# Optimization experiments

Hardware: AMD Instinct MI355X
Metric: run time of the kernel (lower is better)

Reference implementation:

```python
import jax, jax.numpy as jnp
import numpy as np

EPS = 1e-5  # torch BatchNorm2d default eps

def _bn_train(x, g, b):
    # BatchNorm2d in training mode: batch statistics over (N, H, W), biased variance
    m = x.mean(axis=(0, 2, 3), keepdims=True)
    v = x.var(axis=(0, 2, 3), keepdims=True)
    return g[None, :, None, None] * (x - m) / jnp.sqrt(v + EPS) + b[None, :, None, None]

def _conv3(x, w, b):
    y = jax.lax.conv_general_dilated(x, w, (1, 1), 'SAME',
                                     dimension_numbers=('NCHW', 'OIHW', 'NCHW'))
    return y + b[None, :, None, None]

def _conv1(x, w, b):
    # 1x1 conv == per-pixel matmul; w: [out, in]
    return jnp.einsum('bchw,oc->bohw', x, w) + b[None, :, None, None]

def _projector(x, w1, b1, g1, be1, w2, b2, g2, be2):
    h = jax.nn.relu(_bn_train(_conv3(x, w1, b1), g1, be1))
    return _bn_train(_conv1(h, w2, b2), g2, be2)

def _cross_teacher_attention(s, teachers, wq, bq, wk, bk, wv, bv):
    B, C, H, W = s.shape
    scale = C ** -0.5
    q = _conv1(s, wq, bq).reshape(B, C, H * W).transpose(0, 2, 1)  # [B, HW, C]
    outs, ws = [], []
    for t in teachers:  # small fixed list of teachers (structural branch)
        k = _conv1(t, wk, bk).reshape(B, C, H * W).transpose(0, 2, 1)
        v = _conv1(t, wv, bv).reshape(B, C, H * W).transpose(0, 2, 1)
        a = jax.nn.softmax(jnp.einsum('bqc,bkc->bqk', q, k) * scale, axis=-1)  # [B, HW, HW]
        outs.append(jnp.einsum('bqk,bkc->bqc', a, v))                          # [B, HW, C]
        ws.append(a.mean(axis=-1))                                             # [B, HW]
    w = jax.nn.softmax(jnp.stack(ws, axis=-1), axis=-1)          # [B, HW, T]
    fused = jnp.einsum('bqt,tbqc->bqc', w, jnp.stack(outs, 0))   # weighted sum over teachers
    fused = fused.reshape(B, H, W, C).transpose(0, 3, 1, 2)      # [B, C, H, W]
    return s + fused

def setup_inputs() -> dict:
    key = jax.random.key(0)
    ks = jax.random.split(key, 16)
    B, C, H, W = 8, 128, 56, 56
    T = 256  # teacher projector output dim
    d = {}
    d['student_mid'] = jax.random.normal(ks[0], (B, C, H, W), jnp.float32)
    d['t1_mid'] = jax.random.normal(ks[1], (B, C, H, W), jnp.float32)
    d['t2_mid'] = jax.random.normal(ks[2], (B, C, H, W), jnp.float32)
    for i, n in enumerate(['q', 'k', 'v']):
        d['w' + n] = jax.random.normal(ks[3 + i], (C, C), jnp.float32) * 0.05
        d['b' + n] = jnp.zeros((C,), jnp.float32)
    for p, off in (('p1', 6), ('p2', 10)):
        d[p + '_w1'] = jax.random.normal(ks[off], (C, C, 3, 3), jnp.float32) * 0.05
        d[p + '_b1'] = jnp.zeros((C,), jnp.float32)
        d[p + '_g1'] = jnp.ones((C,), jnp.float32)
        d[p + '_be1'] = jnp.zeros((C,), jnp.float32)
        d[p + '_w2'] = jax.random.normal(ks[off + 1], (T, C), jnp.float32) * 0.05
        d[p + '_b2'] = jnp.zeros((T,), jnp.float32)
        d[p + '_g2'] = jnp.ones((T,), jnp.float32)
        d[p + '_be2'] = jnp.zeros((T,), jnp.float32)
    return d

def reference(student_mid, t1_mid, t2_mid, wq, bq, wk, bk, wv, bv,
              p1_w1, p1_b1, p1_g1, p1_be1, p1_w2, p1_b2, p1_g2, p1_be2,
              p2_w1, p2_b1, p2_g1, p2_be1, p2_w2, p2_b2, p2_g2, p2_be2):
    # Per-teacher projectors: computed by the torch module but their outputs are
    # never consumed by the attention (s_feat_proj is unused) -> dead code.
    _sp1 = _projector(student_mid, p1_w1, p1_b1, p1_g1, p1_be1, p1_w2, p1_b2, p1_g2, p1_be2)
    _sp2 = _projector(student_mid, p2_w1, p2_b1, p2_g1, p2_be1, p2_w2, p2_b2, p2_g2, p2_be2)
    del _sp1, _sp2
    return _cross_teacher_attention(student_mid, [t1_mid, t2_mid], wq, bq, wk, bk, wv, bv)
```

## Files before the change

kernel.cpp:

```cpp
#include <hip/hip_runtime.h>

#define HW 3136
#define NB 8
#define CD 128
#define QSCALE 0.12751750206f

typedef __attribute__((ext_vector_type(8))) short short8;
typedef __attribute__((ext_vector_type(4))) float floatx4;
typedef __attribute__((ext_vector_type(4))) unsigned short ushort4v;

static __device__ __forceinline__ unsigned short f2b(float f){
  union { float f; unsigned u; } v; v.f = f;
  unsigned r = v.u + 0x7FFFu + ((v.u >> 16) & 1u);
  return (unsigned short)(r >> 16);
}
static __device__ __forceinline__ float b2f(unsigned short h){
  union { unsigned u; float f; } v; v.u = ((unsigned)h) << 16;
  return v.f;
}

__global__ __launch_bounds__(256) void proj_kernel(
    const float* __restrict__ s, const float* __restrict__ t1, const float* __restrict__ t2,
    const float* __restrict__ wq, const float* __restrict__ bq,
    const float* __restrict__ wk, const float* __restrict__ bk,
    const float* __restrict__ wv, const float* __restrict__ bv,
    unsigned short* __restrict__ qkv)
{
  __shared__ __align__(16) unsigned short WL[CD][136];
  __shared__ __align__(16) unsigned short xsT[64][136];
  const int job = blockIdx.z;
  const float* x; const float* w; const float* bias; float scl; int cmajor; size_t dstoff;
  switch(job){
    case 0: x=s;  w=wq; bias=bq; scl=QSCALE; cmajor=0; dstoff=0; break;
    case 1: x=t1; w=wk; bias=bk; scl=1.f;    cmajor=0; dstoff=1; break;
    case 2: x=t1; w=wv; bias=bv; scl=1.f;    cmajor=1; dstoff=2; break;
    case 3: x=t2; w=wk; bias=bk; scl=1.f;    cmajor=0; dstoff=3; break;
    default:x=t2; w=wv; bias=bv; scl=1.f;    cmajor=1; dstoff=4; break;
  }
  const size_t TS = (size_t)NB*HW*CD;
  const int b   = blockIdx.y;
  const int hw0 = blockIdx.x * 64;
  const int tid = threadIdx.x;

  for (int i = 0; i < 16; i++){
    int flat = tid + i*256;
    int o = flat >> 5, cq = (flat & 31)*4;
    floatx4 wv4 = *(const floatx4*)(w + (size_t)o*CD + cq);
    ushort4v pk;
    for (int j=0;j<4;j++) pk[j] = f2b(wv4[j]);
    *(ushort4v*)&WL[o][cq] = pk;
  }
  const float* xb = x + (size_t)b*CD*HW + hw0;
  for (int i = 0; i < 8; i++){
    int flat = (tid + i*256)*4;
    int c = flat >> 6, hh = flat & 63;
    floatx4 xv = *(const floatx4*)(xb + (size_t)c*HW + hh);
    for (int j=0;j<4;j++) xsT[hh+j][c] = f2b(xv[j]);
  }
  __syncthreads();

  const int m = tid & 15, quad = (tid >> 4) & 3, wv_ = tid >> 6;
  short8 af[4];
  for (int dk=0;dk<4;dk++)
    af[dk] = *(const short8*)&xsT[wv_*16 + m][dk*32 + quad*8];
  float bb[8];
  for (int nt=0;nt<8;nt++) bb[nt] = bias[nt*16 + m];

  unsigned short* dstK = qkv + dstoff*TS + ((size_t)b*HW + hw0)*CD;
  unsigned short* dstV = qkv + dstoff*TS + (size_t)b*CD*HW;
  for (int nt=0;nt<8;nt++){
    floatx4 acc = {bb[nt],bb[nt],bb[nt],bb[nt]};
    for (int dk=0;dk<4;dk++){
      short8 bf = *(const short8*)&WL[nt*16 + m][dk*32 + quad*8];
      acc = __builtin_amdgcn_mfma_f32_16x16x32_bf16(af[dk], bf, acc, 0,0,0);
    }
    if (!cmajor){
      for (int r=0;r<4;r++)
        dstK[(size_t)(wv_*16 + quad*4 + r)*CD + nt*16 + m] = f2b(acc[r]*scl);
    } else {
      ushort4v pk;
      for (int r=0;r<4;r++) pk[r] = f2b(acc[r]*scl);
      *(ushort4v*)&dstV[(size_t)(nt*16 + m)*HW + hw0 + wv_*16 + quad*4] = pk;
    }
  }
}

#define KL_E (64*136)
#define VL_E (128*72)

__global__ __launch_bounds__(256,4) void attn_kernel(
    const unsigned short* __restrict__ qkv,
    unsigned short* __restrict__ Og)
{
  __shared__ __align__(16) unsigned short smem[KL_E + VL_E];
  unsigned short (*Kl)[136] = (unsigned short(*)[136])smem;
  unsigned short (*Vl)[72]  = (unsigned short(*)[72])(smem + KL_E);

  const int qt = blockIdx.x;
  const int b  = blockIdx.y;
  const int t  = blockIdx.z;
  const size_t TS = (size_t)NB*HW*CD;
  const unsigned short* Q = qkv + (size_t)b*HW*CD;
  const unsigned short* K = qkv + TS*(size_t)(1 + 2*t) + (size_t)b*HW*CD;
  const unsigned short* V = qkv + TS*(size_t)(2 + 2*t) + (size_t)b*CD*HW;

  const int tid  = threadIdx.x;
  const int wv_  = tid >> 6;
  const int lane = tid & 63;
  const int m    = lane & 15;
  const int quad = lane >> 4;
  const int q0   = qt*64 + wv_*16;

  short8 qf[4];
  {
    const unsigned short* qr = Q + (size_t)(q0+m)*CD + quad*8;
    for (int dk=0;dk<4;dk++) qf[dk] = *(const short8*)(qr + dk*32);
  }
  floatx4 Oc[8];
  for (int i=0;i<8;i++) Oc[i] = (floatx4)0.f;
  float lr = 0.f;

  const unsigned short* kg = K + (size_t)(tid>>4)*CD + (tid&15)*8;
  const unsigned short* vg = V + (size_t)(tid>>3)*HW + (tid&7)*8;
  unsigned short* klds = &Kl[tid>>4][(tid&15)*8];
  unsigned short* vlds = &Vl[tid>>3][(tid&7)*8];

  short8 kpre[4], vpre[4];
  for (int i=0;i<4;i++) kpre[i] = *(const short8*)(kg + (size_t)i*16*CD);
  for (int i=0;i<4;i++) vpre[i] = *(const short8*)(vg + (size_t)i*32*HW);

  const int sl0 = (((quad<<1)    ) & 3)*16 + m;
  const int sl1 = (((quad<<1) + 1) & 3)*16 + m;
  const bool hiq = (quad >= 2);

  for (int kt = 0; kt < HW/64; kt++){
    __syncthreads();
    for (int i=0;i<4;i++) *(short8*)(klds + i*16*136) = kpre[i];
    for (int i=0;i<4;i++) *(short8*)(vlds + i*32*72)  = vpre[i];
    __syncthreads();
    if (kt < HW/64 - 1){
      kg += 64*CD; vg += 64;
      for (int i=0;i<4;i++) kpre[i] = *(const short8*)(kg + (size_t)i*16*CD);
      for (int i=0;i<4;i++) vpre[i] = *(const short8*)(vg + (size_t)i*32*HW);
    }

    unsigned pw[8];
    for (int nt=0;nt<4;nt++){
      floatx4 acc = (floatx4)0.f;
      for (int dk=0;dk<4;dk++){
        short8 kf = *(const short8*)&Kl[nt*16 + m][dk*32 + quad*8];
        acc = __builtin_amdgcn_mfma_f32_16x16x32_bf16(kf, qf[dk], acc, 0,0,0);
      }
      union { float f; unsigned u; } c0, c1, c2, c3;
      c0.f = __builtin_amdgcn_exp2f(acc[0]);
      c1.f = __builtin_amdgcn_exp2f(acc[1]);
      c2.f = __builtin_amdgcn_exp2f(acc[2]);
      c3.f = __builtin_amdgcn_exp2f(acc[3]);
      lr += (c0.f + c1.f) + (c2.f + c3.f);
      pw[nt*2+0] = (c1.u & 0xFFFF0000u) | (c0.u >> 16);
      pw[nt*2+1] = (c3.u & 0xFFFF0000u) | (c2.u >> 16);
    }

    short8 pf[2];
    for (int kk=0;kk<2;kk++){
      union { unsigned u[4]; short8 s; } bf_;
      for (int w=0;w<4;w++){
        int sl = (w>>1) ? sl1 : sl0;
        int lo = __shfl((int)pw[4*kk     + (w&1)], sl, 64);
        int hi = __shfl((int)pw[4*kk + 2 + (w&1)], sl, 64);
        bf_.u[w] = hiq ? (unsigned)hi : (unsigned)lo;
      }
      pf[kk] = bf_.s;
    }

    for (int ct=0;ct<8;ct++){
      floatx4 o = Oc[ct];
      for (int kk=0;kk<2;kk++){
        short8 vf = *(const short8*)&Vl[ct*16 + m][kk*32 + quad*8];
        o = __builtin_amdgcn_mfma_f32_16x16x32_bf16(vf, pf[kk], o, 0,0,0);
      }
      Oc[ct] = o;
    }
  }

  lr += __shfl_xor(lr, 16, 64);
  lr += __shfl_xor(lr, 32, 64);
  const float inv = 1.f / lr;

  __syncthreads();
  float* stg = ((float*)smem) + wv_*(16*132);
  for (int ct=0;ct<8;ct++){
    floatx4 vv;
    for (int r=0;r<4;r++) vv[r] = Oc[ct][r]*inv;
    *(floatx4*)&stg[m*132 + ct*16 + quad*4] = vv;
  }
  __syncthreads();
  unsigned short* ob = Og + ((size_t)t*NB + b)*HW*CD + (size_t)q0*CD;
  for (int row=0; row<16; row++){
    float v0 = stg[row*132 + 2*lane];
    float v1 = stg[row*132 + 2*lane + 1];
    unsigned short pk[2] = {f2b(v0), f2b(v1)};
    *(unsigned int*)&ob[(size_t)row*CD + 2*lane] = *(const unsigned int*)pk;
  }
}

__global__ __launch_bounds__(256) void combine_kernel(
    const float* __restrict__ s, const unsigned short* __restrict__ Og,
    float* __restrict__ out)
{
  __shared__ float T[32][129];
  const int b   = blockIdx.y;
  const int hw0 = blockIdx.x * 32;
  const int tid = threadIdx.x;
  const unsigned short* O1 = Og + ((size_t)b*HW + hw0)*CD;
  const unsigned short* O2 = O1 + (size_t)NB*HW*CD;
  for (int i=0;i<2;i++){
    int flat = (tid + i*256)*8;
    int row = flat >> 7, col = flat & 127;
    short8 a  = *(const short8*)(O1 + (size_t)row*CD + col);
    short8 c2 = *(const short8*)(O2 + (size_t)row*CD + col);
    for (int j=0;j<8;j++)
      T[row][col+j] = 0.5f*(b2f((unsigned short)a[j]) + b2f((unsigned short)c2[j]));
  }
  __syncthreads();
  const int c  = tid >> 1;
  const int h0 = (tid & 1)*16;
  const float* sr = s   + ((size_t)b*CD + c)*HW + hw0 + h0;
  float*     orow = out + ((size_t)b*CD + c)*HW + hw0 + h0;
  for (int j0=0;j0<16;j0+=4){
    floatx4 sv = *(const floatx4*)(sr + j0);
    floatx4 ov;
    for (int jj=0;jj<4;jj++) ov[jj] = sv[jj] + T[h0+j0+jj][c];
    *(floatx4*)(orow + j0) = ov;
  }
}

extern "C" void kernel_launch(void* const* d_in, const int* in_sizes, int n_in,
                              void* d_out, int out_size, void* d_ws, size_t ws_size,
                              hipStream_t stream)
{
  const float* s  = (const float*)d_in[0];
  const float* t1 = (const float*)d_in[1];
  const float* t2 = (const float*)d_in[2];
  const float* wq = (const float*)d_in[3];
  const float* bq = (const float*)d_in[4];
  const float* wk = (const float*)d_in[5];
  const float* bk = (const float*)d_in[6];
  const float* wv = (const float*)d_in[7];
  const float* bv = (const float*)d_in[8];
  float* out = (float*)d_out;

  unsigned short* qkv = (unsigned short*)d_ws;
  unsigned short* Og  = qkv + (size_t)5*NB*HW*CD;

  hipLaunchKernelGGL(proj_kernel,    dim3(49,8,5), dim3(256), 0, stream,
                     s,t1,t2,wq,bq,wk,bk,wv,bv,qkv);
  hipLaunchKernelGGL(attn_kernel,    dim3(49,8,2), dim3(256), 0, stream, qkv, Og);
  hipLaunchKernelGGL(combine_kernel, dim3(98,8),   dim3(256), 0, stream, s, Og, out);
}
```

Measured before the change: 313.7 us.

## Split attention keys across waves with 16x16x16 MFMA and cross-wave output reduction

Restructures the attention kernel so each wave owns a 16-key slice of every key tile and computes scores for all 64 queries, instead of owning 16 queries and scanning all keys. Because the score accumulator layout now matches the B-operand layout of the 16x16x16 bf16 MFMA, the softmax probabilities feed the PV product directly and the lane-shuffle repacking is gone. The cost is four times more output accumulators per wave (128 floats), a shared-memory reduction of partial outputs and row sums across waves at the end, and occupancy hint lowered from 4 to 2 blocks per CU. The register prefetch of the next K/V tile is also removed, so global loads are no longer overlapped with compute.

```diff
diff --git a/kernel.cpp b/kernel.cpp
--- a/kernel.cpp
+++ b/kernel.cpp
@@ -3,9 +3,11 @@
 #define HW 3136
 #define NB 8
 #define CD 128
+#define NT (HW/64)
 #define QSCALE 0.12751750206f
 
 typedef __attribute__((ext_vector_type(8))) short short8;
+typedef __attribute__((ext_vector_type(4))) short short4v;
 typedef __attribute__((ext_vector_type(4))) float floatx4;
 typedef __attribute__((ext_vector_type(4))) unsigned short ushort4v;
 
@@ -18,6 +20,20 @@
   union { unsigned u; float f; } v; v.u = ((unsigned)h) << 16;
   return v.f;
 }
+
+#if __has_builtin(__builtin_amdgcn_mfma_f32_16x16x16bf16_1k)
+#define MFMA16(a,b,c) __builtin_amdgcn_mfma_f32_16x16x16bf16_1k(a,b,c,0,0,0)
+#elif __has_builtin(__builtin_amdgcn_mfma_f32_16x16x16_bf16)
+#define MFMA16(a,b,c) __builtin_amdgcn_mfma_f32_16x16x16_bf16(a,b,c,0,0,0)
+#else
+static __device__ __forceinline__ floatx4 mfma16_asm(short4v a, short4v b, floatx4 c){
+  floatx4 d;
+  asm volatile("v_mfma_f32_16x16x16_bf16 %0, %1, %2, %3\n\ts_nop 7\n\ts_nop 7"
+               : "=v"(d) : "v"(a), "v"(b), "v"(c));
+  return d;
+}
+#define MFMA16(a,b,c) mfma16_asm(a,b,c)
+#endif
 
 __global__ __launch_bounds__(256) void proj_kernel(
     const float* __restrict__ s, const float* __restrict__ t1, const float* __restrict__ t2,
@@ -87,14 +103,17 @@
 
 #define KL_E (64*136)
 #define VL_E (128*72)
-
-__global__ __launch_bounds__(256,4) void attn_kernel(
+#define SMEM_SH (18432 + 512 + 128)
+
+__global__ __launch_bounds__(256,2) void attn_kernel(
     const unsigned short* __restrict__ qkv,
     unsigned short* __restrict__ Og)
 {
-  __shared__ __align__(16) unsigned short smem[KL_E + VL_E];
+  __shared__ __align__(16) unsigned short smem[SMEM_SH];
   unsigned short (*Kl)[136] = (unsigned short(*)[136])smem;
   unsigned short (*Vl)[72]  = (unsigned short(*)[72])(smem + KL_E);
+  float* lrb  = (float*)(smem + 18432);
+  float* invL = (float*)(smem + 18432 + 512);
 
   const int qt = blockIdx.x;
   const int b  = blockIdx.y;
@@ -109,98 +128,117 @@
   const int lane = tid & 63;
   const int m    = lane & 15;
   const int quad = lane >> 4;
-  const int q0   = qt*64 + wv_*16;
-
-  short8 qf[4];
-  {
-    const unsigned short* qr = Q + (size_t)(q0+m)*CD + quad*8;
-    for (int dk=0;dk<4;dk++) qf[dk] = *(const short8*)(qr + dk*32);
-  }
-  floatx4 Oc[8];
-  for (int i=0;i<8;i++) Oc[i] = (floatx4)0.f;
-  float lr = 0.f;
+  const int q0   = qt*64;
+
+  short8 qf[4][4];
+#pragma unroll
+  for (int qs=0;qs<4;qs++){
+    const unsigned short* qr = Q + (size_t)(q0 + qs*16 + m)*CD + quad*8;
+#pragma unroll
+    for (int dk=0;dk<4;dk++) qf[qs][dk] = *(const short8*)(qr + dk*32);
+  }
+
+  floatx4 Oc[8][4];
+#pragma unroll
+  for (int i=0;i<8;i++)
+#pragma unroll
+    for (int j=0;j<4;j++) Oc[i][j] = (floatx4)0.f;
+  float lr[4] = {0.f,0.f,0.f,0.f};
 
   const unsigned short* kg = K + (size_t)(tid>>4)*CD + (tid&15)*8;
   const unsigned short* vg = V + (size_t)(tid>>3)*HW + (tid&7)*8;
   unsigned short* klds = &Kl[tid>>4][(tid&15)*8];
   unsigned short* vlds = &Vl[tid>>3][(tid&7)*8];
 
-  short8 kpre[4], vpre[4];
-  for (int i=0;i<4;i++) kpre[i] = *(const short8*)(kg + (size_t)i*16*CD);
-  for (int i=0;i<4;i++) vpre[i] = *(const short8*)(vg + (size_t)i*32*HW);
-
-  const int sl0 = (((quad<<1)    ) & 3)*16 + m;
-  const int sl1 = (((quad<<1) + 1) & 3)*16 + m;
-  const bool hiq = (quad >= 2);
-
-  for (int kt = 0; kt < HW/64; kt++){
+  for (int kt = 0; kt < NT; kt++){
+    short8 kr[4], vr[4];
+#pragma unroll
+    for (int i=0;i<4;i++) kr[i] = *(const short8*)(kg + (size_t)i*16*CD);
+#pragma unroll
+    for (int i=0;i<4;i++) vr[i] = *(const short8*)(vg + (size_t)i*32*HW);
+    kg += 64*CD; vg += 64;
+    if (kt) __syncthreads();
+#pragma unroll
+    for (int i=0;i<4;i++) *(short8*)(klds + i*16*136) = kr[i];
+#pragma unroll
+    for (int i=0;i<4;i++) *(short8*)(vlds + i*32*72)  = vr[i];
     __syncthreads();
-    for (int i=0;i<4;i++) *(short8*)(klds + i*16*136) = kpre[i];
-    for (int i=0;i<4;i++) *(short8*)(vlds + i*32*72)  = vpre[i];
-    __syncthreads();
-    if (kt < HW/64 - 1){
-      kg += 64*CD; vg += 64;
-      for (int i=0;i<4;i++) kpre[i] = *(const short8*)(kg + (size_t)i*16*CD);
-      for (int i=0;i<4;i++) vpre[i] = *(const short8*)(vg + (size_t)i*32*HW);
-    }
-
-    unsigned pw[8];
-    for (int nt=0;nt<4;nt++){
+
+    short8 af[4];
+#pragma unroll
+    for (int dk=0;dk<4;dk++)
+      af[dk] = *(const short8*)&Kl[wv_*16 + m][dk*32 + quad*8];
+
+    short4v pfv[4];
+#pragma unroll
+    for (int qs=0;qs<4;qs++){
       floatx4 acc = (floatx4)0.f;
-      for (int dk=0;dk<4;dk++){
-        short8 kf = *(const short8*)&Kl[nt*16 + m][dk*32 + quad*8];
-        acc = __builtin_amdgcn_mfma_f32_16x16x32_bf16(kf, qf[dk], acc, 0,0,0);
-      }
+#pragma unroll
+      for (int dk=0;dk<4;dk++)
+        acc = __builtin_amdgcn_mfma_f32_16x16x32_bf16(af[dk], qf[qs][dk], acc, 0,0,0);
       union { float f; unsigned u; } c0, c1, c2, c3;
       c0.f = __builtin_amdgcn_exp2f(acc[0]);
       c1.f = __builtin_amdgcn_exp2f(acc[1]);
       c2.f = __builtin_amdgcn_exp2f(acc[2]);
       c3.f = __builtin_amdgcn_exp2f(acc[3]);
-      lr += (c0.f + c1.f) + (c2.f + c3.f);
-      pw[nt*2+0] = (c1.u & 0xFFFF0000u) | (c0.u >> 16);
-      pw[nt*2+1] = (c3.u & 0xFFFF0000u) | (c2.u >> 16);
-    }
-
-    short8 pf[2];
-    for (int kk=0;kk<2;kk++){
-      union { unsigned u[4]; short8 s; } bf_;
-      for (int w=0;w<4;w++){
-        int sl = (w>>1) ? sl1 : sl0;
-        int lo = __shfl((int)pw[4*kk     + (w&1)], sl, 64);
-        int hi = __shfl((int)pw[4*kk + 2 + (w&1)], sl, 64);
-        bf_.u[w] = hiq ? (unsigned)hi : (unsigned)lo;
-      }
-      pf[kk] = bf_.s;
-    }
-
+      lr[qs] += (c0.f + c1.f) + (c2.f + c3.f);
+      union { unsigned u[2]; short4v s; } pk;
+      pk.u[0] = (c1.u & 0xFFFF0000u) | (c0.u >> 16);
+      pk.u[1] = (c3.u & 0xFFFF0000u) | (c2.u >> 16);
+      pfv[qs] = pk.s;
+    }
+
+#pragma unroll
     for (int ct=0;ct<8;ct++){
-      floatx4 o = Oc[ct];
-      for (int kk=0;kk<2;kk++){
-        short8 vf = *(const short8*)&Vl[ct*16 + m][kk*32 + quad*8];
-        o = __builtin_amdgcn_mfma_f32_16x16x32_bf16(vf, pf[kk], o, 0,0,0);
-      }
-      Oc[ct] = o;
-    }
-  }
-
-  lr += __shfl_xor(lr, 16, 64);
-  lr += __shfl_xor(lr, 32, 64);
-  const float inv = 1.f / lr;
-
-  __syncthreads();
-  float* stg = ((float*)smem) + wv_*(16*132);
-  for (int ct=0;ct<8;ct++){
-    floatx4 vv;
-    for (int r=0;r<4;r++) vv[r] = Oc[ct][r]*inv;
-    *(floatx4*)&stg[m*132 + ct*16 + quad*4] = vv;
-  }
-  __syncthreads();
+      short4v vf = *(const short4v*)&Vl[ct*16 + m][wv_*16 + quad*4];
+#pragma unroll
+      for (int qs=0;qs<4;qs++)
+        Oc[ct][qs] = MFMA16(vf, pfv[qs], Oc[ct][qs]);
+    }
+  }
+
+#pragma unroll
+  for (int qs=0;qs<4;qs++){
+    lr[qs] += __shfl_xor(lr[qs], 16, 64);
+    lr[qs] += __shfl_xor(lr[qs], 32, 64);
+  }
+  if (quad == 0){
+#pragma unroll
+    for (int qs=0;qs<4;qs++) lrb[wv_*64 + qs*16 + m] = lr[qs];
+  }
+  __syncthreads();
+  if (tid < 64)
+    invL[tid] = 1.f/(lrb[tid] + lrb[64+tid] + lrb[128+tid] + lrb[192+tid]);
+  __syncthreads();
+
+  float* Of = (float*)smem;
   unsigned short* ob = Og + ((size_t)t*NB + b)*HW*CD + (size_t)q0*CD;
-  for (int row=0; row<16; row++){
-    float v0 = stg[row*132 + 2*lane];
-    float v1 = stg[row*132 + 2*lane + 1];
-    unsigned short pk[2] = {f2b(v0), f2b(v1)};
-    *(unsigned int*)&ob[(size_t)row*CD + 2*lane] = *(const unsigned int*)pk;
+  const int qlr = wv_*16 + (lane>>2);
+  const int c8  = (lane&3)*8;
+#pragma unroll
+  for (int rd=0; rd<4; rd++){
+#pragma unroll
+    for (int cc=0; cc<2; cc++){
+#pragma unroll
+      for (int qs=0; qs<4; qs++)
+        *(floatx4*)&Of[wv_*2304 + (qs*16+m)*36 + cc*16 + quad*4] = Oc[rd*2+cc][qs];
+    }
+    __syncthreads();
+    floatx4 s0 = (floatx4)0.f, s1 = (floatx4)0.f;
+#pragma unroll
+    for (int w=0; w<4; w++){
+      s0 += *(const floatx4*)&Of[w*2304 + qlr*36 + c8];
+      s1 += *(const floatx4*)&Of[w*2304 + qlr*36 + c8 + 4];
+    }
+    float iv = invL[qlr];
+    short8 o;
+#pragma unroll
+    for (int j=0;j<4;j++){
+      o[j]   = (short)f2b(s0[j]*iv);
+      o[4+j] = (short)f2b(s1[j]*iv);
+    }
+    *(short8*)&ob[(size_t)qlr*CD + rd*32 + c8] = o;
+    __syncthreads();
   }
 }
 
```

After: 287.4 us. -8.4%, faster.
